# Optimization experiments

Measured on AMD Instinct MI355X. Metric: run time of the kernel, lower is better.

Reference implementation:

```python
import jax, jax.numpy as jnp
import numpy as np

B, H, W, C = 2, 128, 128, 192
HEADS = 6
HD = C // HEADS
WS = 16
OWIN = int(WS * 0.5) + WS          # 24
PAD = (OWIN - WS) // 2             # 4
NQ = WS * WS
NK = OWIN * OWIN
EPS = 1e-6
HID = ((int(C * 2.667) + 7) // 8) * 8  # 512


def _rel_pos_index():
    cq = np.stack(np.meshgrid(np.arange(WS), np.arange(WS), indexing='ij')).reshape(2, -1)
    ck = np.stack(np.meshgrid(np.arange(OWIN), np.arange(OWIN), indexing='ij')).reshape(2, -1)
    rel = (ck[:, None, :] - cq[:, :, None]).transpose(1, 2, 0).astype(np.int64)  # (nq, nk, 2)
    rel[:, :, 0] += WS - 1
    rel[:, :, 1] += WS - 1
    rel[:, :, 0] *= WS + OWIN - 1
    return rel.sum(-1)  # (nq, nk)

RPI = jnp.asarray(_rel_pos_index())


def setup_inputs() -> dict:
    key = jax.random.key(0)
    ks = jax.random.split(key, 16)
    def w(k, shape, s=0.02):
        return jax.random.normal(k, shape, jnp.float32) * s
    return {
        'x': jax.random.normal(ks[0], (B, H * W, C), jnp.float32),
        'qkv_w': w(ks[1], (3 * C, C)), 'qkv_b': jnp.zeros((3 * C,), jnp.float32),
        'proj_w': w(ks[2], (C, C)), 'proj_b': jnp.zeros((C,), jnp.float32),
        'rpb': w(ks[3], ((WS + OWIN - 1) ** 2, HEADS)),
        'n1_w': jnp.ones((C,), jnp.float32), 'n1_b': jnp.zeros((C,), jnp.float32),
        'ls1': jnp.full((C,), 1e-6, jnp.float32),
        'n2_w': jnp.ones((C,), jnp.float32), 'n2_b': jnp.zeros((C,), jnp.float32),
        'ls2': jnp.full((C,), 1e-6, jnp.float32),
        'fcgv_w': w(ks[4], (2 * HID, C)), 'fcgv_b': jnp.zeros((2 * HID,), jnp.float32),
        'dw_w': w(ks[5], (HID, 1, 3, 3)), 'dw_b': jnp.zeros((HID,), jnp.float32),
        'dwd_w': w(ks[6], (HID, 1, 3, 3)), 'dwd_b': jnp.zeros((HID,), jnp.float32),
        'dil_scale': w(ks[7], (1,), 0.1),
        'fco_w': w(ks[8], (C, HID)), 'fco_b': jnp.zeros((C,), jnp.float32),
    }


def _iln(x, wgt, bias):
    # spatially-holistic LN: stats over (L, C); returns normed x and residual scale
    xf = x.astype(jnp.float32)
    mean = xf.mean(axis=(1, 2), keepdims=True)
    var = ((xf - mean) ** 2).mean(axis=(1, 2), keepdims=True)
    std = jnp.sqrt(var + EPS)
    scale = jnp.minimum(std, 2.0)  # std_ema buffer initialized to 1.0 (eval path)
    xn = (xf - mean) / scale
    return (xn * wgt + bias).astype(x.dtype), scale


def _oca(x, qkv_w, qkv_b, proj_w, proj_b, rpb):
    b = x.shape[0]
    nh, nw = H // WS, W // WS
    nwin = b * nh * nw
    qkv = x @ qkv_w.T + qkv_b
    q, k, v = jnp.split(qkv, 3, axis=-1)
    # non-overlapping query windows: (nwin, heads, nq, hd)
    qw = q.reshape(b, nh, WS, nw, WS, C).transpose(0, 1, 3, 2, 4, 5)
    qw = qw.reshape(nwin, NQ, HEADS, HD).transpose(0, 2, 1, 3)
    # overlapping K/V windows via unfold(kernel=OWIN, stride=WS, pad=PAD)
    kv = jnp.concatenate([k, v], axis=-1).reshape(b, H, W, 2 * C).transpose(0, 3, 1, 2)
    kvp = jnp.pad(kv, ((0, 0), (0, 0), (PAD, PAD), (PAD, PAD)))
    ih = (jnp.arange(nh) * WS)[:, None] + jnp.arange(OWIN)[None, :]
    iw = (jnp.arange(nw) * WS)[:, None] + jnp.arange(OWIN)[None, :]
    kvw = kvp[:, :, ih][:, :, :, :, iw]               # (b, 2C, nh, owin, nw, owin)
    kvw = kvw.transpose(0, 2, 4, 3, 5, 1).reshape(nwin, NK, 2 * C)
    kw = kvw[..., :C].reshape(nwin, NK, HEADS, HD).transpose(0, 2, 1, 3)
    vw = kvw[..., C:].reshape(nwin, NK, HEADS, HD).transpose(0, 2, 1, 3)
    bias = rpb[RPI].transpose(2, 0, 1)                # (heads, nq, nk)
    logits = jnp.einsum('whqd,whkd->whqk', qw, kw) * (HD ** -0.5) + bias
    attn = jax.nn.softmax(logits, axis=-1)
    out = jnp.einsum('whqk,whkd->whqd', attn, vw)
    out = out.transpose(0, 2, 1, 3).reshape(nwin, NQ, C) @ proj_w.T + proj_b
    # window reverse -> (b, H*W, C)
    out = out.reshape(b, nh, nw, WS, WS, C).transpose(0, 1, 3, 2, 4, 5).reshape(b, H * W, C)
    return out


def _dw(x, wgt, bias, dil):
    y = jax.lax.conv_general_dilated(x, wgt, (1, 1), [(dil, dil), (dil, dil)],
                                     rhs_dilation=(dil, dil), feature_group_count=HID)
    return y + bias[None, :, None, None]


def _ffn(x, fcgv_w, fcgv_b, dw_w, dw_b, dwd_w, dwd_b, dil_scale, fco_w, fco_b):
    gv = x @ fcgv_w.T + fcgv_b
    g, val = jnp.split(gv, 2, axis=-1)
    h = jax.nn.silu(g) * val
    h = h.transpose(0, 2, 1).reshape(-1, HID, H, W)
    h = _dw(h, dw_w, dw_b, 1)
    h = h + dil_scale[0] * _dw(h, dwd_w, dwd_b, 2)
    h = h.reshape(-1, HID, H * W).transpose(0, 2, 1)
    return h @ fco_w.T + fco_b


def reference(x, qkv_w, qkv_b, proj_w, proj_b, rpb, n1_w, n1_b, ls1, n2_w, n2_b, ls2,
              fcgv_w, fcgv_b, dw_w, dw_b, dwd_w, dwd_b, dil_scale, fco_w, fco_b):
    xn, std1 = _iln(x, n1_w, n1_b)
    x = x + std1 * (ls1 * _oca(xn, qkv_w, qkv_b, proj_w, proj_b, rpb))
    xn2, std2 = _iln(x, n2_w, n2_b)
    x = x + std2 * (ls2 * _ffn(xn2, fcgv_w, fcgv_b, dw_w, dw_b, dwd_w, dwd_b, dil_scale, fco_w, fco_b))
    return x
```

## Files before the change

kernel.cpp:

```cpp
#include <hip/hip_runtime.h>

#define DI __device__ __forceinline__

typedef __attribute__((ext_vector_type(8))) short bh8;
typedef __attribute__((ext_vector_type(4))) float fx4;
typedef __attribute__((ext_vector_type(16))) float fx16;

DI short f2bf(float f) {
  unsigned u = __builtin_bit_cast(unsigned, f);
  u += 0x7FFFu + ((u >> 16) & 1u);
  return (short)(u >> 16);
}
DI float bf2f(short s) {
  unsigned u = ((unsigned)(unsigned short)s) << 16;
  return __builtin_bit_cast(float, u);
}
DI fx4 mfma16(bh8 a, bh8 b, fx4 c) {
  return __builtin_amdgcn_mfma_f32_16x16x32_bf16(a, b, c, 0, 0, 0);
}
DI fx16 mfma32(bh8 a, bh8 b, fx16 c) {
  return __builtin_amdgcn_mfma_f32_32x32x16_bf16(a, b, c, 0, 0, 0);
}
DI fx4 fzero() { fx4 z = {0.f, 0.f, 0.f, 0.f}; return z; }

DI float fexp2(float x) {
#if __has_builtin(__builtin_amdgcn_exp2f)
  return __builtin_amdgcn_exp2f(x);
#else
  return exp2f(x);
#endif
}

DI bh8 pack8(const float* src) {
  fx4 v0 = *(const fx4*)src;
  fx4 v1 = *(const fx4*)(src + 4);
  bh8 pk;
#pragma unroll
  for (int j = 0; j < 4; j++) { pk[j] = f2bf(v0[j]); pk[j + 4] = f2bf(v1[j]); }
  return pk;
}
DI bh8 pack8_aff(const float* src, const float* affc) {
  fx4 v0 = *(const fx4*)src;
  fx4 v1 = *(const fx4*)(src + 4);
  bh8 pk;
#pragma unroll
  for (int j = 0; j < 4; j++) {
    pk[j]     = f2bf(v0[j] * affc[2 * j]       + affc[2 * j + 1]);
    pk[j + 4] = f2bf(v1[j] * affc[2 * (j + 4)] + affc[2 * (j + 4) + 1]);
  }
  return pk;
}

__global__ __launch_bounds__(256) void iln_partial(const float* __restrict__ x,
                                                   float* __restrict__ part) {
  const int blk = blockIdx.x, tid = threadIdx.x;
  const fx4* p = (const fx4*)(x + (size_t)blk * 12288);
  float s = 0.f, s2 = 0.f;
#pragma unroll
  for (int i = 0; i < 12; i++) {
    fx4 v = p[i * 256 + tid];
    s  += v[0] + v[1] + v[2] + v[3];
    s2 += v[0] * v[0] + v[1] * v[1] + v[2] * v[2] + v[3] * v[3];
  }
  __shared__ float sm[512];
  sm[tid] = s; sm[256 + tid] = s2;
  __syncthreads();
  for (int st = 128; st > 0; st >>= 1) {
    if (tid < st) { sm[tid] += sm[tid + st]; sm[256 + tid] += sm[256 + tid + st]; }
    __syncthreads();
  }
  if (tid == 0) { part[blk * 2] = sm[0]; part[blk * 2 + 1] = sm[256]; }
}

__global__ __launch_bounds__(256) void iln_final(const float* __restrict__ part,
                                                 const float* __restrict__ w,
                                                 const float* __restrict__ bias,
                                                 float* __restrict__ aff,
                                                 float* __restrict__ st) {
  const int b = blockIdx.x, tid = threadIdx.x;
  __shared__ float sm[512];
  sm[tid]       = part[(b * 256 + tid) * 2];
  sm[256 + tid] = part[(b * 256 + tid) * 2 + 1];
  __syncthreads();
  for (int s = 128; s > 0; s >>= 1) {
    if (tid < s) { sm[tid] += sm[tid + s]; sm[256 + tid] += sm[256 + tid + s]; }
    __syncthreads();
  }
  const float invn = 1.f / 3145728.f;
  float mean = sm[0] * invn;
  float var  = sm[256] * invn - mean * mean;
  float scale = fminf(sqrtf(var + 1e-6f), 2.f);
  if (tid < 192) {
    float a = w[tid] / scale;
    aff[(b * 192 + tid) * 2]     = a;
    aff[(b * 192 + tid) * 2 + 1] = bias[tid] - mean * a;
  }
  if (tid == 0) { st[b * 2] = mean; st[b * 2 + 1] = scale; }
}

__global__ __launch_bounds__(256) void cvt_w(const float* __restrict__ qkv_w,
                                             const float* __restrict__ proj_w,
                                             const float* __restrict__ fcgv_w,
                                             const float* __restrict__ fco_w,
                                             short* __restrict__ wbuf) {
  int t = blockIdx.x * 256 + threadIdx.x;
  int blk = t >> 6, lane = t & 63;
  int g = lane >> 4, h = lane & 15;
  const float* src;
  if (blk < 216) {
    int b2 = blk;
    int ni = b2 % 3; b2 /= 3;
    int wn = b2 & 1; b2 >>= 1;
    int kt = b2 % 6; b2 /= 6;
    int nt = b2;
    src = qkv_w + (size_t)(nt * 96 + wn * 48 + ni * 16 + h) * 192 + kt * 32 + g * 8;
  } else if (blk < 288) {
    int b2 = blk - 216;
    int ni = b2 % 3; b2 /= 3;
    int wn = b2 & 1; b2 >>= 1;
    int kt = b2 % 6; b2 /= 6;
    int nt = b2;
    src = proj_w + (size_t)(nt * 96 + wn * 48 + ni * 16 + h) * 192 + kt * 32 + g * 8;
  } else if (blk < 672) {
    int b2 = blk - 288;
    int gv = b2 & 1; b2 >>= 1;
    int ni = b2 & 1; b2 >>= 1;
    int wn = b2 & 1; b2 >>= 1;
    int kt = b2 % 6; b2 /= 6;
    int nt = b2;
    int r = wn * 32 + ni * 16 + h;
    int row = gv ? (512 + nt * 64 + r) : (nt * 64 + r);
    src = fcgv_w + (size_t)row * 192 + kt * 32 + g * 8;
  } else {
    int b2 = blk - 672;
    int ni = b2 % 3; b2 /= 3;
    int wn = b2 & 1; b2 >>= 1;
    int kt = b2 & 15; b2 >>= 4;
    int nt = b2;
    src = fco_w + (size_t)(nt * 96 + wn * 48 + ni * 16 + h) * 512 + kt * 32 + g * 8;
  }
  *(bh8*)(wbuf + (size_t)blk * 512 + lane * 8) = pack8(src);
}

__global__ __launch_bounds__(256) void cvt_aff(const float* __restrict__ src,
                                               const float* __restrict__ aff,
                                               short* __restrict__ dst) {
  int t = blockIdx.x * 256 + threadIdx.x;
  int row = t / 24;
  int c0 = (t - row * 24) * 8;
  const float* affp = aff + (row >> 14) * 384 + c0 * 2;
  int mt = row >> 7, wm = (row >> 6) & 1, mi = (row >> 4) & 3, h = row & 15;
  int kt = c0 >> 5, g = (c0 >> 3) & 3;
  int blk = ((mt * 2 + wm) * 4 + mi) * 6 + kt;
  int lane = g * 16 + h;
  *(bh8*)(dst + (size_t)blk * 512 + lane * 8) = pack8_aff(src + (size_t)row * 192 + c0, affp);
}

__global__ __launch_bounds__(256) void bias_gen(const float* __restrict__ rpb,
                                                float* __restrict__ btf) {
  int t = blockIdx.x * 256 + threadIdx.x;
  int lane = t & 63;
  int u = t >> 6;
  int qi = u & 1; int u2 = u >> 1;
  int ki = u2 & 1; u2 >>= 1;
  int kc = u2 % 9; u2 = u2 / 9;
  int w = u2 & 3, head = u2 >> 2;
  int c = lane & 31, hi = lane >> 5;
  int q = w * 64 + qi * 32 + c;
  int qterm = (q >> 4) * 39 + (q & 15);
  (void)ki; (void)kc;
  float o[16];
#pragma unroll
  for (int r = 0; r < 16; r++) {
    int kk = ((u >> 2) % 9) * 64 + ((u >> 1) & 1) * 32 + (r & 3) + 8 * (r >> 2) + 4 * hi;
    int ky = (kk * 2731) >> 16;
    int kx = kk - ky * 24;
    int idx = ky * 39 + kx + 600 - qterm;
    o[r] = rpb[idx * 6 + head] * 1.4426950408889634f;
  }
  fx4* dst = (fx4*)btf;
#pragma unroll
  for (int j = 0; j < 4; j++) {
    fx4 v = {o[4 * j], o[4 * j + 1], o[4 * j + 2], o[4 * j + 3]};
    dst[((size_t)u * 4 + j) * 64 + lane] = v;
  }
}

__global__ __launch_bounds__(256) void gemm_qkv(const short* __restrict__ xn,
                                                const short* __restrict__ wq,
                                                const float* __restrict__ wb,
                                                short* __restrict__ qb,
                                                short* __restrict__ kb,
                                                short* __restrict__ vb) {
  const int mt = blockIdx.x, by = blockIdx.y;
  const int m0 = mt * 128;
  const int tid = threadIdx.x, wid = tid >> 6, lane = tid & 63;
  const int g = lane >> 4, h = lane & 15;
  const int wm = wid >> 1, wn = wid & 1;
  fx4 acc[4][3];
#pragma unroll
  for (int i = 0; i < 4; i++)
#pragma unroll
    for (int j = 0; j < 3; j++) acc[i][j] = fzero();

#pragma unroll
  for (int kt = 0; kt < 6; kt++) {
    bh8 af[4], bf[3];
#pragma unroll
    for (int mi = 0; mi < 4; mi++)
      af[mi] = *(const bh8*)(xn + (size_t)((((mt * 2 + wm) * 4 + mi) * 6 + kt)) * 512 + lane * 8);
#pragma unroll
    for (int ni = 0; ni < 3; ni++)
      bf[ni] = *(const bh8*)(wq + (size_t)(((by * 6 + kt) * 2 + wn) * 3 + ni) * 512 + lane * 8);
#pragma unroll
    for (int ni = 0; ni < 3; ni++)
#pragma unroll
      for (int mi = 0; mi < 4; mi++) acc[mi][ni] = mfma16(af[mi], bf[ni], acc[mi][ni]);
  }
  const int seg = by >> 1;
  short* dst = (seg == 0) ? qb : (seg == 1 ? kb : vb);
  const float sc = (seg == 1) ? 0.25503486f : 1.0f;
  const int colbase = (by & 1) * 96;
#pragma unroll
  for (int mi = 0; mi < 4; mi++)
#pragma unroll
    for (int ni = 0; ni < 3; ni++)
#pragma unroll
      for (int r = 0; r < 4; r++) {
        int row = m0 + wm * 64 + mi * 16 + g * 4 + r;
        int col = colbase + wn * 48 + ni * 16 + h;
        dst[(size_t)row * 192 + col] = f2bf((acc[mi][ni][r] + wb[seg * 192 + col]) * sc);
      }
}

__global__ __launch_bounds__(256, 3) void attn_kernel(const short* __restrict__ qb,
                                                      const short* __restrict__ kb,
                                                      const short* __restrict__ vb,
                                                      const float* __restrict__ btf,
                                                      short* __restrict__ ao) {
  __shared__ short K_lds[64 * 40];
  __shared__ short Vt_lds[32 * 72];
  __shared__ float l_lds[256];
  const int tid = threadIdx.x;
  const int win = blockIdx.x, head = blockIdx.y;
  const int b = win >> 6, wy = (win >> 3) & 7, wx = win & 7;
  const int w = tid >> 6, lane = tid & 63, c = lane & 31, hi = lane >> 5;

  bh8 qf[2][2];
#pragma unroll
  for (int qi = 0; qi < 2; qi++) {
    int ql = w * 64 + qi * 32 + c;
    size_t gl = (size_t)(b * 16384 + (wy * 16 + (ql >> 4)) * 128 + wx * 16 + (ql & 15));
#pragma unroll
    for (int ds = 0; ds < 2; ds++)
      qf[qi][ds] = *(const bh8*)(qb + gl * 192 + head * 32 + ds * 16 + hi * 8);
  }
  float l_run[2] = {0.f, 0.f};
  fx16 out[2];
#pragma unroll
  for (int r = 0; r < 16; r++) { out[0][r] = 0.f; out[1][r] = 0.f; }

  const fx4* btf4 = (const fx4*)btf;
  const int hw9 = (head * 4 + w) * 9;

  const int kl_a = tid >> 2, part_a = tid & 3;
  const int kl_b = tid & 63, hg_b = tid >> 6;

  for (int kc = 0; kc < 9; kc++) {
    __syncthreads();
    {
      int key = kc * 64 + kl_a;
      int ky = key / 24, kx = key - ky * 24;
      int py = wy * 16 - 4 + ky, px = wx * 16 - 4 + kx;
      bh8 kv = {};
      if ((unsigned)py < 128u && (unsigned)px < 128u)
        kv = *(const bh8*)(kb + ((size_t)(b * 16384 + py * 128 + px)) * 192 + head * 32 + part_a * 8);
      *(bh8*)&K_lds[kl_a * 40 + part_a * 8] = kv;

      int key2 = kc * 64 + kl_b;
      int ky2 = key2 / 24, kx2 = key2 - ky2 * 24;
      int py2 = wy * 16 - 4 + ky2, px2 = wx * 16 - 4 + kx2;
      bh8 vv = {};
      if ((unsigned)py2 < 128u && (unsigned)px2 < 128u)
        vv = *(const bh8*)(vb + ((size_t)(b * 16384 + py2 * 128 + px2)) * 192 + head * 32 + hg_b * 8);
#pragma unroll
      for (int j = 0; j < 8; j++) Vt_lds[(hg_b * 8 + j) * 72 + kl_b] = vv[j];
    }
    __syncthreads();

    const fx4* base_kc = btf4 + (size_t)(hw9 + kc) * 1024 + lane;
#pragma unroll
    for (int ki = 0; ki < 2; ki++) {
      fx16 st[2];
#pragma unroll
      for (int qi = 0; qi < 2; qi++) {
        const fx4* bp = base_kc + (ki * 2 + qi) * 256;
        fx4 b0 = bp[0], b1 = bp[64], b2 = bp[128], b3 = bp[192];
#pragma unroll
        for (int m = 0; m < 4; m++) {
          st[qi][m]      = b0[m];
          st[qi][4 + m]  = b1[m];
          st[qi][8 + m]  = b2[m];
          st[qi][12 + m] = b3[m];
        }
      }
      __builtin_amdgcn_s_setprio(1);
#pragma unroll
      for (int ds = 0; ds < 2; ds++) {
        bh8 kf = *(bh8*)&K_lds[(ki * 32 + c) * 40 + ds * 16 + hi * 8];
        st[0] = mfma32(kf, qf[0][ds], st[0]);
        st[1] = mfma32(kf, qf[1][ds], st[1]);
      }
      __builtin_amdgcn_s_setprio(0);
#pragma unroll
      for (int qi = 0; qi < 2; qi++) {
        float s = 0.f;
#pragma unroll
        for (int r = 0; r < 16; r++) {
          float p = fexp2(st[qi][r]);
          st[qi][r] = p;
          s += p;
        }
        l_run[qi] += s;
      }
      int dwq[2][2][4];
#pragma unroll
      for (int qi = 0; qi < 2; qi++)
#pragma unroll
        for (int k1 = 0; k1 < 2; k1++)
#pragma unroll
          for (int p01 = 0; p01 < 2; p01++) {
            int rA = 2 * p01 + 8 * k1;
            int A, Bv;
            asm("v_cvt_pk_bf16_f32 %0, %1, %2" : "=v"(A)  : "v"(st[qi][rA]),     "v"(st[qi][rA + 1]));
            asm("v_cvt_pk_bf16_f32 %0, %1, %2" : "=v"(Bv) : "v"(st[qi][rA + 4]), "v"(st[qi][rA + 5]));
#if __has_builtin(__builtin_amdgcn_permlane32_swap)
            auto pr = __builtin_amdgcn_permlane32_swap((unsigned)A, (unsigned)Bv, false, false);
            dwq[qi][k1][p01]     = (int)pr[0];
            dwq[qi][k1][p01 + 2] = (int)pr[1];
#else
            int Ax = __shfl_xor(A, 32);
            int Bx = __shfl_xor(Bv, 32);
            dwq[qi][k1][p01]     = hi ? Bx : A;
            dwq[qi][k1][p01 + 2] = hi ? Bv : Ax;
#endif
          }
      __builtin_amdgcn_s_setprio(1);
#pragma unroll
      for (int k1 = 0; k1 < 2; k1++) {
        bh8 bv2 = *(bh8*)&Vt_lds[c * 72 + (ki * 2 + k1) * 16 + hi * 8];
#pragma unroll
        for (int qi = 0; qi < 2; qi++) {
          int4 t4 = {dwq[qi][k1][0], dwq[qi][k1][1], dwq[qi][k1][2], dwq[qi][k1][3]};
          out[qi] = mfma32(__builtin_bit_cast(bh8, t4), bv2, out[qi]);
        }
      }
      __builtin_amdgcn_s_setprio(0);
    }
  }
#pragma unroll
  for (int qi = 0; qi < 2; qi++) {
    float lp = l_run[qi] + __shfl_xor(l_run[qi], 32);
    l_lds[w * 64 + qi * 32 + c] = 1.f / lp;
  }
  __syncthreads();
#pragma unroll
  for (int qi = 0; qi < 2; qi++)
#pragma unroll
    for (int r = 0; r < 16; r++) {
      int row = (r & 3) + 8 * (r >> 2) + 4 * hi;
      float val = out[qi][r] * l_lds[w * 64 + qi * 32 + row];
      int ql = w * 64 + qi * 32 + row;
      ao[((size_t)(win * 256 + ql)) * 192 + head * 32 + c] = f2bf(val);
    }
}

__global__ __launch_bounds__(256) void gemm_proj(const short* __restrict__ ao,
                                                 const short* __restrict__ wp,
                                                 const float* __restrict__ wb,
                                                 const float* __restrict__ x,
                                                 const float* __restrict__ ls1,
                                                 const float* __restrict__ st,
                                                 float* __restrict__ x1,
                                                 float* __restrict__ part2) {
  __shared__ float red[512];
  const int m0 = blockIdx.x * 128, by = blockIdx.y;
  const int tid = threadIdx.x, wid = tid >> 6, lane = tid & 63;
  const int g = lane >> 4, h = lane & 15;
  const int wm = wid >> 1, wn = wid & 1;
  fx4 acc[4][3];
#pragma unroll
  for (int i = 0; i < 4; i++)
#pragma unroll
    for (int j = 0; j < 3; j++) acc[i][j] = fzero();

#pragma unroll
  for (int kt = 0; kt < 6; kt++) {
    bh8 af[4], bf[3];
#pragma unroll
    for (int mi = 0; mi < 4; mi++)
      af[mi] = *(const bh8*)(ao + (size_t)(m0 + wm * 64 + mi * 16 + h) * 192 + kt * 32 + g * 8);
#pragma unroll
    for (int ni = 0; ni < 3; ni++)
      bf[ni] = *(const bh8*)(wp + (size_t)(((by * 6 + kt) * 2 + wn) * 3 + ni) * 512 + lane * 8);
#pragma unroll
    for (int ni = 0; ni < 3; ni++)
#pragma unroll
      for (int mi = 0; mi < 4; mi++) acc[mi][ni] = mfma16(af[mi], bf[ni], acc[mi][ni]);
  }
  const int n0 = by * 96;
  float ps = 0.f, ps2 = 0.f;
#pragma unroll
  for (int mi = 0; mi < 4; mi++)
#pragma unroll
    for (int ni = 0; ni < 3; ni++)
#pragma unroll
      for (int r = 0; r < 4; r++) {
        int grow = m0 + wm * 64 + mi * 16 + g * 4 + r;
        int win = grow >> 8, q = grow & 255;
        int bb = win >> 6, wy = (win >> 3) & 7, wxx = win & 7;
        int l = (wy * 16 + (q >> 4)) * 128 + wxx * 16 + (q & 15);
        int col = n0 + wn * 48 + ni * 16 + h;
        size_t di = ((size_t)(bb * 16384 + l)) * 192 + col;
        float s1 = st[bb * 2 + 1];
        float val = x[di] + s1 * ls1[col] * (acc[mi][ni][r] + wb[col]);
        x1[di] = val;
        ps += val;
        ps2 += val * val;
      }
  red[tid] = ps; red[256 + tid] = ps2;
  __syncthreads();
  for (int s = 128; s > 0; s >>= 1) {
    if (tid < s) { red[tid] += red[tid + s]; red[256 + tid] += red[256 + tid + s]; }
    __syncthreads();
  }
  if (tid == 0) {
    int pi = blockIdx.x * 2 + by;
    part2[pi * 2] = red[0];
    part2[pi * 2 + 1] = red[256];
  }
}

__global__ __launch_bounds__(256) void gemm_fcgv(const short* __restrict__ x1n,
                                                 const short* __restrict__ wg,
                                                 const float* __restrict__ wb,
                                                 short* __restrict__ hp) {
  __shared__ short T[64 * 136];
  const int mt = blockIdx.x, by = blockIdx.y, n0 = by * 64;
  const int m0 = mt * 128;
  const int b = m0 >> 14, l0 = m0 & 16383;
  const int tid = threadIdx.x, wid = tid >> 6, lane = tid & 63;
  const int g = lane >> 4, h = lane & 15;
  const int wm = wid >> 1, wn = wid & 1;
  fx4 accg[4][2], accv[4][2];
#pragma unroll
  for (int i = 0; i < 4; i++)
#pragma unroll
    for (int j = 0; j < 2; j++) { accg[i][j] = fzero(); accv[i][j] = fzero(); }

#pragma unroll
  for (int kt = 0; kt < 6; kt++) {
    bh8 af[4], bg[2], bv[2];
#pragma unroll
    for (int mi = 0; mi < 4; mi++)
      af[mi] = *(const bh8*)(x1n + (size_t)((((mt * 2 + wm) * 4 + mi) * 6 + kt)) * 512 + lane * 8);
#pragma unroll
    for (int ni = 0; ni < 2; ni++) {
      size_t base = (size_t)((((by * 6 + kt) * 2 + wn) * 2 + ni) * 2) * 512;
      bg[ni] = *(const bh8*)(wg + base + lane * 8);
      bv[ni] = *(const bh8*)(wg + base + 512 + lane * 8);
    }
#pragma unroll
    for (int ni = 0; ni < 2; ni++)
#pragma unroll
      for (int mi = 0; mi < 4; mi++) {
        accg[mi][ni] = mfma16(af[mi], bg[ni], accg[mi][ni]);
        accv[mi][ni] = mfma16(af[mi], bv[ni], accv[mi][ni]);
      }
  }
  short hs[4][2][4];
#pragma unroll
  for (int mi = 0; mi < 4; mi++)
#pragma unroll
    for (int ni = 0; ni < 2; ni++)
#pragma unroll
      for (int r = 0; r < 4; r++) {
        int colg = n0 + wn * 32 + ni * 16 + h;
        float gv = accg[mi][ni][r] + wb[colg];
        float vv = accv[mi][ni][r] + wb[512 + colg];
        hs[mi][ni][r] = f2bf(gv / (1.f + __expf(-gv)) * vv);
      }
#pragma unroll
  for (int mi = 0; mi < 4; mi++)
#pragma unroll
    for (int ni = 0; ni < 2; ni++)
#pragma unroll
      for (int r = 0; r < 4; r++) {
        int cc = wn * 32 + ni * 16 + h;
        int rl = wm * 64 + mi * 16 + g * 4 + r;
        T[cc * 136 + rl] = hs[mi][ni][r];
      }
  __syncthreads();
#pragma unroll
  for (int i = 0; i < 4; i++) {
    int ch = tid + i * 256;
    int cc = ch >> 4, lg = ch & 15;
    bh8 v = *(bh8*)&T[cc * 136 + lg * 8];
    *(bh8*)(hp + (((size_t)(b * 512 + n0 + cc)) << 14) + l0 + lg * 8) = v;
  }
}

__global__ __launch_bounds__(256) void dw_fused(const short* __restrict__ in,
                                                const float* __restrict__ w1,
                                                const float* __restrict__ b1,
                                                const float* __restrict__ w2,
                                                const float* __restrict__ b2,
                                                const float* __restrict__ dsc,
                                                short* __restrict__ outp) {
  __shared__ short P[70 * 136];
  __shared__ short D[68 * 136];
  const int p = blockIdx.x >> 1, s = blockIdx.x & 1, c = p & 511;
  const int tid = threadIdx.x;
  const int r0 = s * 64;
  const int plo = s ? 61 : 0;
  const int pbase = r0 - 3;
  const int dlo = s ? 62 : 0;
  const int dbase = r0 - 2;
  const short* ip = in + ((size_t)p << 14);

  for (int i = tid; i < 67 * 16; i += 256) {
    int rr = plo + (i >> 4), sl = i & 15;
    bh8 v = *(const bh8*)(ip + rr * 128 + sl * 8);
    *(bh8*)&P[(rr - pbase) * 136 + sl * 8] = v;
  }
  float k1[9], k2[9];
#pragma unroll
  for (int j = 0; j < 9; j++) { k1[j] = w1[c * 9 + j]; k2[j] = w2[c * 9 + j]; }
  const float bias1 = b1[c], bias2 = b2[c], ds = dsc[0];
  __syncthreads();

  for (int i = tid; i < 66 * 16; i += 256) {
    int gy = dlo + (i >> 4);
    int x0 = (i & 15) * 8;
    float acc[8];
#pragma unroll
    for (int q = 0; q < 8; q++) acc[q] = bias1;
#pragma unroll
    for (int ky = 0; ky < 3; ky++) {
      int yy = gy + ky - 1;
      if ((unsigned)yy < 128u) {
        const short* row = &P[(yy - pbase) * 136];
        float f[10];
        bh8 v = *(const bh8*)&row[x0];
#pragma unroll
        for (int j = 0; j < 8; j++) f[j + 1] = bf2f(v[j]);
        f[0] = (x0 == 0) ? 0.f : bf2f(row[x0 - 1]);
        f[9] = (x0 == 120) ? 0.f : bf2f(row[x0 + 8]);
        float w0 = k1[ky * 3], wA = k1[ky * 3 + 1], wB = k1[ky * 3 + 2];
#pragma unroll
        for (int q = 0; q < 8; q++) acc[q] += f[q] * w0 + f[q + 1] * wA + f[q + 2] * wB;
      }
    }
    bh8 pk;
#pragma unroll
    for (int q = 0; q < 8; q++) pk[q] = f2bf(acc[q]);
    *(bh8*)&D[(gy - dbase) * 136 + x0] = pk;
  }
  __syncthreads();

  for (int i = tid; i < 64 * 16; i += 256) {
    int gy = r0 + (i >> 4);
    int x0 = (i & 15) * 8;
    float acc[8], center[8];
#pragma unroll
    for (int q = 0; q < 8; q++) acc[q] = bias2;
#pragma unroll
    for (int ky = 0; ky < 3; ky++) {
      int yy = gy + (ky - 1) * 2;
      if ((unsigned)yy < 128u) {
        const short* row = &D[(yy - dbase) * 136];
        float f[12];
        bh8 v = *(const bh8*)&row[x0];
#pragma unroll
        for (int j = 0; j < 8; j++) f[j + 2] = bf2f(v[j]);
        if (x0 == 0) { f[0] = 0.f; f[1] = 0.f; }
        else {
          unsigned lp = *(const unsigned*)&row[x0 - 2];
          f[0] = __builtin_bit_cast(float, lp << 16);
          f[1] = __builtin_bit_cast(float, lp & 0xffff0000u);
        }
        if (x0 == 120) { f[10] = 0.f; f[11] = 0.f; }
        else {
          unsigned rp = *(const unsigned*)&row[x0 + 8];
          f[10] = __builtin_bit_cast(float, rp << 16);
          f[11] = __builtin_bit_cast(float, rp & 0xffff0000u);
        }
        float w0 = k2[ky * 3], wA = k2[ky * 3 + 1], wB = k2[ky * 3 + 2];
#pragma unroll
        for (int q = 0; q < 8; q++) acc[q] += f[q] * w0 + f[q + 2] * wA + f[q + 4] * wB;
        if (ky == 1) {
#pragma unroll
          for (int q = 0; q < 8; q++) center[q] = f[q + 2];
        }
      }
    }
    bh8 pk;
#pragma unroll
    for (int q = 0; q < 8; q++) pk[q] = f2bf(center[q] + ds * acc[q]);
    *(bh8*)(outp + ((size_t)p << 14) + gy * 128 + x0) = pk;
  }
}

__global__ __launch_bounds__(256) void gemm_fco(const short* __restrict__ h2,
                                                const short* __restrict__ wo,
                                                const float* __restrict__ wb,
                                                const float* __restrict__ x1,
                                                const float* __restrict__ ls2,
                                                const float* __restrict__ st,
                                                float* __restrict__ out) {
  __shared__ short As[128 * 40];
  const int m0 = blockIdx.x * 128, by = blockIdx.y, n0 = by * 96;
  const int b = m0 >> 14, l0 = m0 & 16383;
  const int tid = threadIdx.x, wid = tid >> 6, lane = tid & 63;
  const int g = lane >> 4, h = lane & 15;
  const int wm = wid >> 1, wn = wid & 1;
  const int cp = tid & 15, lg = tid >> 4;
  fx4 acc[4][3];
#pragma unroll
  for (int i = 0; i < 4; i++)
#pragma unroll
    for (int j = 0; j < 3; j++) acc[i][j] = fzero();

  for (int kt = 0; kt < 16; kt++) {
    const int k0 = kt * 32;
    {
      const short* basep = h2 + (((size_t)(b * 512 + k0 + 2 * cp)) << 14) + l0 + lg * 8;
      bh8 v0 = *(const bh8*)basep;
      bh8 v1 = *(const bh8*)(basep + 16384);
#pragma unroll
      for (int j = 0; j < 8; j++) {
        unsigned pkv = (unsigned)(unsigned short)v0[j] | (((unsigned)(unsigned short)v1[j]) << 16);
        *(unsigned*)&As[(lg * 8 + j) * 40 + 2 * cp] = pkv;
      }
    }
    __syncthreads();
    bh8 af[4], bf[3];
#pragma unroll
    for (int mi = 0; mi < 4; mi++)
      af[mi] = *(bh8*)&As[(wm * 64 + mi * 16 + h) * 40 + g * 8];
#pragma unroll
    for (int ni = 0; ni < 3; ni++)
      bf[ni] = *(const bh8*)(wo + (size_t)(((by * 16 + kt) * 2 + wn) * 3 + ni) * 512 + lane * 8);
#pragma unroll
    for (int ni = 0; ni < 3; ni++)
#pragma unroll
      for (int mi = 0; mi < 4; mi++) acc[mi][ni] = mfma16(af[mi], bf[ni], acc[mi][ni]);
    __syncthreads();
  }
  float s2 = st[b * 2 + 1];
#pragma unroll
  for (int mi = 0; mi < 4; mi++)
#pragma unroll
    for (int ni = 0; ni < 3; ni++)
#pragma unroll
      for (int r = 0; r < 4; r++) {
        int row = m0 + wm * 64 + mi * 16 + g * 4 + r;
        int col = n0 + wn * 48 + ni * 16 + h;
        size_t di = (size_t)row * 192 + col;
        out[di] = x1[di] + s2 * ls2[col] * (acc[mi][ni][r] + wb[col]);
      }
}

extern "C" void kernel_launch(void* const* d_in, const int* in_sizes, int n_in,
                              void* d_out, int out_size, void* d_ws, size_t ws_size,
                              hipStream_t stream) {
  const float* x      = (const float*)d_in[0];
  const float* qkv_w  = (const float*)d_in[1];
  const float* qkv_b  = (const float*)d_in[2];
  const float* proj_w = (const float*)d_in[3];
  const float* proj_b = (const float*)d_in[4];
  const float* rpb    = (const float*)d_in[5];
  const float* n1_w   = (const float*)d_in[6];
  const float* n1_b   = (const float*)d_in[7];
  const float* ls1    = (const float*)d_in[8];
  const float* n2_w   = (const float*)d_in[9];
  const float* n2_b   = (const float*)d_in[10];
  const float* ls2    = (const float*)d_in[11];
  const float* fcgv_w = (const float*)d_in[12];
  const float* fcgv_b = (const float*)d_in[13];
  const float* dw_w   = (const float*)d_in[14];
  const float* dw_b   = (const float*)d_in[15];
  const float* dwd_w  = (const float*)d_in[16];
  const float* dwd_b  = (const float*)d_in[17];
  const float* dil    = (const float*)d_in[18];
  const float* fco_w  = (const float*)d_in[19];
  const float* fco_b  = (const float*)d_in[20];
  float* out = (float*)d_out;
  char* ws = (char*)d_ws;

  short* wbuf = (short*)(ws + 0);
  short* wq = wbuf;
  short* wp = wbuf + 110592;
  short* wg = wbuf + 147456;
  short* wo = wbuf + 344064;
  float* part  = (float*)(ws + 884736);
  float* aff1  = (float*)(ws + 888832);
  float* aff2  = (float*)(ws + 890368);
  float* st1   = (float*)(ws + 891904);
  float* st2   = (float*)(ws + 891968);
  float* part2 = (float*)(ws + 892032);
  short* xn  = (short*)(ws + 1048576);
  float* btf = (float*)(ws + 13631488);
  short* qb  = (short*)(ws + 17301504);
  short* kb  = (short*)(ws + 29884416);
  short* vb  = (short*)(ws + 42467328);
  short* ao  = (short*)(ws + 55050240);
  float* x1  = (float*)(ws + 1048576);
  short* x1n = (short*)(ws + 26214400);
  short* hp  = (short*)(ws + 42467328);
  short* h2  = (short*)(ws + 76021760);

  cvt_w<<<216, 256, 0, stream>>>(qkv_w, proj_w, fcgv_w, fco_w, wbuf);
  iln_partial<<<512, 256, 0, stream>>>(x, part);
  iln_final<<<2, 256, 0, stream>>>(part, n1_w, n1_b, aff1, st1);
  cvt_aff<<<3072, 256, 0, stream>>>(x, aff1, xn);
  bias_gen<<<216, 256, 0, stream>>>(rpb, btf);
  gemm_qkv<<<dim3(256, 6), 256, 0, stream>>>(xn, wq, qkv_b, qb, kb, vb);
  attn_kernel<<<dim3(128, 6), 256, 0, stream>>>(qb, kb, vb, btf, ao);
  gemm_proj<<<dim3(256, 2), 256, 0, stream>>>(ao, wp, proj_b, x, ls1, st1, x1, part2);
  iln_final<<<2, 256, 0, stream>>>(part2, n2_w, n2_b, aff2, st2);
  cvt_aff<<<3072, 256, 0, stream>>>(x1, aff2, x1n);
  gemm_fcgv<<<dim3(256, 8), 256, 0, stream>>>(x1n, wg, fcgv_b, hp);
  dw_fused<<<2048, 256, 0, stream>>>(hp, dw_w, dw_b, dwd_w, dwd_b, dil, h2);
  gemm_fco<<<dim3(256, 2), 256, 0, stream>>>(h2, wo, fco_b, x1, ls2, st2, out);
}
```

Baseline: 186.7 us.

## Fuse prep kernels, fold LN finalize into cvt_aff, store attention bias as bf16

Merges the weight conversion and relative-position bias generation into one prep launch. The two iln_final launches are removed: every cvt_aff block now reduces the partial sums itself to get mean and scale. The precomputed attention bias table is stored in bf16 instead of fp32, which halves the bias bytes the attention kernel reads per key chunk. The cost is redundant reduction work in each of the 3072 cvt_aff blocks and lower precision in the bias added to the logits.

```diff
diff --git a/kernel.cpp b/kernel.cpp
--- a/kernel.cpp
+++ b/kernel.cpp
@@ -39,17 +39,6 @@
   for (int j = 0; j < 4; j++) { pk[j] = f2bf(v0[j]); pk[j + 4] = f2bf(v1[j]); }
   return pk;
 }
-DI bh8 pack8_aff(const float* src, const float* affc) {
-  fx4 v0 = *(const fx4*)src;
-  fx4 v1 = *(const fx4*)(src + 4);
-  bh8 pk;
-#pragma unroll
-  for (int j = 0; j < 4; j++) {
-    pk[j]     = f2bf(v0[j] * affc[2 * j]       + affc[2 * j + 1]);
-    pk[j + 4] = f2bf(v1[j] * affc[2 * (j + 4)] + affc[2 * (j + 4) + 1]);
-  }
-  return pk;
-}
 
 __global__ __launch_bounds__(256) void iln_partial(const float* __restrict__ x,
                                                    float* __restrict__ part) {
@@ -72,118 +61,122 @@
   if (tid == 0) { part[blk * 2] = sm[0]; part[blk * 2 + 1] = sm[256]; }
 }
 
-__global__ __launch_bounds__(256) void iln_final(const float* __restrict__ part,
-                                                 const float* __restrict__ w,
-                                                 const float* __restrict__ bias,
-                                                 float* __restrict__ aff,
-                                                 float* __restrict__ st) {
-  const int b = blockIdx.x, tid = threadIdx.x;
-  __shared__ float sm[512];
-  sm[tid]       = part[(b * 256 + tid) * 2];
-  sm[256 + tid] = part[(b * 256 + tid) * 2 + 1];
+__global__ __launch_bounds__(256) void prep(const float* __restrict__ qkv_w,
+                                            const float* __restrict__ proj_w,
+                                            const float* __restrict__ fcgv_w,
+                                            const float* __restrict__ fco_w,
+                                            const float* __restrict__ rpb,
+                                            short* __restrict__ wbuf,
+                                            short* __restrict__ btb) {
+  if (blockIdx.x < 216) {
+    int t = blockIdx.x * 256 + threadIdx.x;
+    int blk = t >> 6, lane = t & 63;
+    int g = lane >> 4, h = lane & 15;
+    const float* src;
+    if (blk < 216) {
+      int b2 = blk;
+      int ni = b2 % 3; b2 /= 3;
+      int wn = b2 & 1; b2 >>= 1;
+      int kt = b2 % 6; b2 /= 6;
+      int nt = b2;
+      src = qkv_w + (size_t)(nt * 96 + wn * 48 + ni * 16 + h) * 192 + kt * 32 + g * 8;
+    } else if (blk < 288) {
+      int b2 = blk - 216;
+      int ni = b2 % 3; b2 /= 3;
+      int wn = b2 & 1; b2 >>= 1;
+      int kt = b2 % 6; b2 /= 6;
+      int nt = b2;
+      src = proj_w + (size_t)(nt * 96 + wn * 48 + ni * 16 + h) * 192 + kt * 32 + g * 8;
+    } else if (blk < 672) {
+      int b2 = blk - 288;
+      int gv = b2 & 1; b2 >>= 1;
+      int ni = b2 & 1; b2 >>= 1;
+      int wn = b2 & 1; b2 >>= 1;
+      int kt = b2 % 6; b2 /= 6;
+      int nt = b2;
+      int r = wn * 32 + ni * 16 + h;
+      int row = gv ? (512 + nt * 64 + r) : (nt * 64 + r);
+      src = fcgv_w + (size_t)row * 192 + kt * 32 + g * 8;
+    } else {
+      int b2 = blk - 672;
+      int ni = b2 % 3; b2 /= 3;
+      int wn = b2 & 1; b2 >>= 1;
+      int kt = b2 & 15; b2 >>= 4;
+      int nt = b2;
+      src = fco_w + (size_t)(nt * 96 + wn * 48 + ni * 16 + h) * 512 + kt * 32 + g * 8;
+    }
+    *(bh8*)(wbuf + (size_t)blk * 512 + lane * 8) = pack8(src);
+  } else {
+    int t = (blockIdx.x - 216) * 256 + threadIdx.x;
+    int lane = t & 63;
+    int u = t >> 6;
+    int qi = u & 1;
+    int c = lane & 31, hi = lane >> 5;
+    int w = (u >> 2) / 9 % 4;
+    int head = (u >> 2) / 36;
+    int q = w * 64 + qi * 32 + c;
+    int qterm = (q >> 4) * 39 + (q & 15);
+    short o16[16];
+#pragma unroll
+    for (int r = 0; r < 16; r++) {
+      int kk = ((u >> 2) % 9) * 64 + ((u >> 1) & 1) * 32 + (r & 3) + 8 * (r >> 2) + 4 * hi;
+      int ky = (kk * 2731) >> 16;
+      int kx = kk - ky * 24;
+      int idx = ky * 39 + kx + 600 - qterm;
+      o16[r] = f2bf(rpb[idx * 6 + head] * 1.4426950408889634f);
+    }
+    *(bh8*)(btb + (size_t)u * 1024 + lane * 16)     = *(bh8*)&o16[0];
+    *(bh8*)(btb + (size_t)u * 1024 + lane * 16 + 8) = *(bh8*)&o16[8];
+  }
+}
+
+__global__ __launch_bounds__(256) void cvt_aff(const float* __restrict__ src,
+                                               const float* __restrict__ part,
+                                               const float* __restrict__ w,
+                                               const float* __restrict__ bias,
+                                               short* __restrict__ dst,
+                                               float* __restrict__ st) {
+  __shared__ float rs[512];
+  const int tid = threadIdx.x;
+  const int bb = (blockIdx.x >= 1536) ? 1 : 0;
+  rs[tid]       = part[(bb * 256 + tid) * 2];
+  rs[256 + tid] = part[(bb * 256 + tid) * 2 + 1];
   __syncthreads();
   for (int s = 128; s > 0; s >>= 1) {
-    if (tid < s) { sm[tid] += sm[tid + s]; sm[256 + tid] += sm[256 + tid + s]; }
+    if (tid < s) { rs[tid] += rs[tid + s]; rs[256 + tid] += rs[256 + tid + s]; }
     __syncthreads();
   }
   const float invn = 1.f / 3145728.f;
-  float mean = sm[0] * invn;
-  float var  = sm[256] * invn - mean * mean;
+  float mean = rs[0] * invn;
+  float var  = rs[256] * invn - mean * mean;
   float scale = fminf(sqrtf(var + 1e-6f), 2.f);
-  if (tid < 192) {
-    float a = w[tid] / scale;
-    aff[(b * 192 + tid) * 2]     = a;
-    aff[(b * 192 + tid) * 2 + 1] = bias[tid] - mean * a;
-  }
-  if (tid == 0) { st[b * 2] = mean; st[b * 2 + 1] = scale; }
-}
-
-__global__ __launch_bounds__(256) void cvt_w(const float* __restrict__ qkv_w,
-                                             const float* __restrict__ proj_w,
-                                             const float* __restrict__ fcgv_w,
-                                             const float* __restrict__ fco_w,
-                                             short* __restrict__ wbuf) {
-  int t = blockIdx.x * 256 + threadIdx.x;
-  int blk = t >> 6, lane = t & 63;
-  int g = lane >> 4, h = lane & 15;
-  const float* src;
-  if (blk < 216) {
-    int b2 = blk;
-    int ni = b2 % 3; b2 /= 3;
-    int wn = b2 & 1; b2 >>= 1;
-    int kt = b2 % 6; b2 /= 6;
-    int nt = b2;
-    src = qkv_w + (size_t)(nt * 96 + wn * 48 + ni * 16 + h) * 192 + kt * 32 + g * 8;
-  } else if (blk < 288) {
-    int b2 = blk - 216;
-    int ni = b2 % 3; b2 /= 3;
-    int wn = b2 & 1; b2 >>= 1;
-    int kt = b2 % 6; b2 /= 6;
-    int nt = b2;
-    src = proj_w + (size_t)(nt * 96 + wn * 48 + ni * 16 + h) * 192 + kt * 32 + g * 8;
-  } else if (blk < 672) {
-    int b2 = blk - 288;
-    int gv = b2 & 1; b2 >>= 1;
-    int ni = b2 & 1; b2 >>= 1;
-    int wn = b2 & 1; b2 >>= 1;
-    int kt = b2 % 6; b2 /= 6;
-    int nt = b2;
-    int r = wn * 32 + ni * 16 + h;
-    int row = gv ? (512 + nt * 64 + r) : (nt * 64 + r);
-    src = fcgv_w + (size_t)row * 192 + kt * 32 + g * 8;
-  } else {
-    int b2 = blk - 672;
-    int ni = b2 % 3; b2 /= 3;
-    int wn = b2 & 1; b2 >>= 1;
-    int kt = b2 & 15; b2 >>= 4;
-    int nt = b2;
-    src = fco_w + (size_t)(nt * 96 + wn * 48 + ni * 16 + h) * 512 + kt * 32 + g * 8;
-  }
-  *(bh8*)(wbuf + (size_t)blk * 512 + lane * 8) = pack8(src);
-}
-
-__global__ __launch_bounds__(256) void cvt_aff(const float* __restrict__ src,
-                                               const float* __restrict__ aff,
-                                               short* __restrict__ dst) {
-  int t = blockIdx.x * 256 + threadIdx.x;
+  if (tid == 0 && (blockIdx.x == 0 || blockIdx.x == 1536)) {
+    st[bb * 2] = mean;
+    st[bb * 2 + 1] = scale;
+  }
+  const float isc = 1.f / scale;
+  int t = blockIdx.x * 256 + tid;
   int row = t / 24;
   int c0 = (t - row * 24) * 8;
-  const float* affp = aff + (row >> 14) * 384 + c0 * 2;
   int mt = row >> 7, wm = (row >> 6) & 1, mi = (row >> 4) & 3, h = row & 15;
   int kt = c0 >> 5, g = (c0 >> 3) & 3;
   int blk = ((mt * 2 + wm) * 4 + mi) * 6 + kt;
   int lane = g * 16 + h;
-  *(bh8*)(dst + (size_t)blk * 512 + lane * 8) = pack8_aff(src + (size_t)row * 192 + c0, affp);
-}
-
-__global__ __launch_bounds__(256) void bias_gen(const float* __restrict__ rpb,
-                                                float* __restrict__ btf) {
-  int t = blockIdx.x * 256 + threadIdx.x;
-  int lane = t & 63;
-  int u = t >> 6;
-  int qi = u & 1; int u2 = u >> 1;
-  int ki = u2 & 1; u2 >>= 1;
-  int kc = u2 % 9; u2 = u2 / 9;
-  int w = u2 & 3, head = u2 >> 2;
-  int c = lane & 31, hi = lane >> 5;
-  int q = w * 64 + qi * 32 + c;
-  int qterm = (q >> 4) * 39 + (q & 15);
-  (void)ki; (void)kc;
-  float o[16];
-#pragma unroll
-  for (int r = 0; r < 16; r++) {
-    int kk = ((u >> 2) % 9) * 64 + ((u >> 1) & 1) * 32 + (r & 3) + 8 * (r >> 2) + 4 * hi;
-    int ky = (kk * 2731) >> 16;
-    int kx = kk - ky * 24;
-    int idx = ky * 39 + kx + 600 - qterm;
-    o[r] = rpb[idx * 6 + head] * 1.4426950408889634f;
-  }
-  fx4* dst = (fx4*)btf;
+  const float* sp = src + (size_t)row * 192 + c0;
+  fx4 v0 = *(const fx4*)sp;
+  fx4 v1 = *(const fx4*)(sp + 4);
+  bh8 pk;
 #pragma unroll
   for (int j = 0; j < 4; j++) {
-    fx4 v = {o[4 * j], o[4 * j + 1], o[4 * j + 2], o[4 * j + 3]};
-    dst[((size_t)u * 4 + j) * 64 + lane] = v;
-  }
+    float a = w[c0 + j] * isc;
+    pk[j] = f2bf(v0[j] * a + (bias[c0 + j] - mean * a));
+  }
+#pragma unroll
+  for (int j = 0; j < 4; j++) {
+    float a = w[c0 + 4 + j] * isc;
+    pk[j + 4] = f2bf(v1[j] * a + (bias[c0 + 4 + j] - mean * a));
+  }
+  *(bh8*)(dst + (size_t)blk * 512 + lane * 8) = pk;
 }
 
 __global__ __launch_bounds__(256) void gemm_qkv(const short* __restrict__ xn,
@@ -236,7 +229,7 @@
 __global__ __launch_bounds__(256, 3) void attn_kernel(const short* __restrict__ qb,
                                                       const short* __restrict__ kb,
                                                       const short* __restrict__ vb,
-                                                      const float* __restrict__ btf,
+                                                      const short* __restrict__ btb,
                                                       short* __restrict__ ao) {
   __shared__ short K_lds[64 * 40];
   __shared__ short Vt_lds[32 * 72];
@@ -260,7 +253,6 @@
 #pragma unroll
   for (int r = 0; r < 16; r++) { out[0][r] = 0.f; out[1][r] = 0.f; }
 
-  const fx4* btf4 = (const fx4*)btf;
   const int hw9 = (head * 4 + w) * 9;
 
   const int kl_a = tid >> 2, part_a = tid & 3;
@@ -288,20 +280,23 @@
     }
     __syncthreads();
 
-    const fx4* base_kc = btf4 + (size_t)(hw9 + kc) * 1024 + lane;
+    const short* base_kc = btb + (size_t)(hw9 + kc) * 4096 + lane * 16;
 #pragma unroll
     for (int ki = 0; ki < 2; ki++) {
       fx16 st[2];
 #pragma unroll
       for (int qi = 0; qi < 2; qi++) {
-        const fx4* bp = base_kc + (ki * 2 + qi) * 256;
-        fx4 b0 = bp[0], b1 = bp[64], b2 = bp[128], b3 = bp[192];
-#pragma unroll
-        for (int m = 0; m < 4; m++) {
-          st[qi][m]      = b0[m];
-          st[qi][4 + m]  = b1[m];
-          st[qi][8 + m]  = b2[m];
-          st[qi][12 + m] = b3[m];
+        const short* bp = base_kc + (ki * 2 + qi) * 1024;
+        int4 b0 = *(const int4*)bp;
+        int4 b1 = *(const int4*)(bp + 8);
+#pragma unroll
+        for (int d = 0; d < 4; d++) {
+          unsigned u0 = ((const unsigned*)&b0)[d];
+          unsigned u1 = ((const unsigned*)&b1)[d];
+          st[qi][2 * d]     = __builtin_bit_cast(float, u0 << 16);
+          st[qi][2 * d + 1] = __builtin_bit_cast(float, u0 & 0xffff0000u);
+          st[qi][8 + 2 * d]     = __builtin_bit_cast(float, u1 << 16);
+          st[qi][8 + 2 * d + 1] = __builtin_bit_cast(float, u1 & 0xffff0000u);
         }
       }
       __builtin_amdgcn_s_setprio(1);
@@ -704,13 +699,11 @@
   short* wg = wbuf + 147456;
   short* wo = wbuf + 344064;
   float* part  = (float*)(ws + 884736);
-  float* aff1  = (float*)(ws + 888832);
-  float* aff2  = (float*)(ws + 890368);
   float* st1   = (float*)(ws + 891904);
   float* st2   = (float*)(ws + 891968);
   float* part2 = (float*)(ws + 892032);
   short* xn  = (short*)(ws + 1048576);
-  float* btf = (float*)(ws + 13631488);
+  short* btb = (short*)(ws + 13631488);
   short* qb  = (short*)(ws + 17301504);
   short* kb  = (short*)(ws + 29884416);
   short* vb  = (short*)(ws + 42467328);
@@ -720,16 +713,13 @@
   short* hp  = (short*)(ws + 42467328);
   short* h2  = (short*)(ws + 76021760);
 
-  cvt_w<<<216, 256, 0, stream>>>(qkv_w, proj_w, fcgv_w, fco_w, wbuf);
   iln_partial<<<512, 256, 0, stream>>>(x, part);
-  iln_final<<<2, 256, 0, stream>>>(part, n1_w, n1_b, aff1, st1);
-  cvt_aff<<<3072, 256, 0, stream>>>(x, aff1, xn);
-  bias_gen<<<216, 256, 0, stream>>>(rpb, btf);
+  prep<<<432, 256, 0, stream>>>(qkv_w, proj_w, fcgv_w, fco_w, rpb, wbuf, btb);
+  cvt_aff<<<3072, 256, 0, stream>>>(x, part, n1_w, n1_b, xn, st1);
   gemm_qkv<<<dim3(256, 6), 256, 0, stream>>>(xn, wq, qkv_b, qb, kb, vb);
-  attn_kernel<<<dim3(128, 6), 256, 0, stream>>>(qb, kb, vb, btf, ao);
+  attn_kernel<<<dim3(128, 6), 256, 0, stream>>>(qb, kb, vb, btb, ao);
   gemm_proj<<<dim3(256, 2), 256, 0, stream>>>(ao, wp, proj_b, x, ls1, st1, x1, part2);
-  iln_final<<<2, 256, 0, stream>>>(part2, n2_w, n2_b, aff2, st2);
-  cvt_aff<<<3072, 256, 0, stream>>>(x1, aff2, x1n);
+  cvt_aff<<<3072, 256, 0, stream>>>(x1, part2, n2_w, n2_b, x1n, st2);
   gemm_fcgv<<<dim3(256, 8), 256, 0, stream>>>(x1n, wg, fcgv_b, hp);
   dw_fused<<<2048, 256, 0, stream>>>(hp, dw_w, dw_b, dwd_w, dwd_b, dil, h2);
   gemm_fco<<<dim3(256, 2), 256, 0, stream>>>(h2, wo, fco_b, x1, ls2, st2, out);
```

New measurement: 173.6 us (median of 2 runs). 1.08x faster.
